# Performance work log

Hardware: AMD Instinct MI355X
Metric: run time of the kernel (lower is better)

The kernel has to match this reference:

```python
import jax, jax.numpy as jnp
import numpy as np

B, T, F = 64, 1024, 64  # F == K
K_FACTORS = 64
U = 256
GP_ELL = 10.0
GP_NOISE = 0.1


def setup_inputs() -> dict:
    key = jax.random.key(0)
    ks = jax.random.split(key, 5)
    inputs = jax.random.normal(ks[0], (B, T, F), dtype=jnp.float32)
    Wx = jax.random.normal(ks[1], (F, 4 * U), dtype=jnp.float32) * 0.05
    Wh = jax.random.normal(ks[2], (U, 4 * U), dtype=jnp.float32) * 0.05
    b = jnp.zeros((4 * U,), dtype=jnp.float32)
    Wd = jax.random.normal(ks[3], (U, 1), dtype=jnp.float32) * 0.05
    bd = jnp.zeros((1,), dtype=jnp.float32)
    return {"inputs": inputs, "Wx": Wx, "Wh": Wh, "b": b, "Wd": Wd, "bd": bd}


def _lstm(x, Wx, Wh, b):
    # x: (B, T, F) -> hidden sequence (B, T, U). Keras gate order: i, f, g(c), o.
    Bn = x.shape[0]
    Un = Wh.shape[0]
    x_t = jnp.swapaxes(x, 0, 1)  # (T, B, F)
    h0 = jnp.zeros((Bn, Un), x.dtype)
    c0 = jnp.zeros((Bn, Un), x.dtype)

    def step(carry, xt):
        h, c = carry
        z = xt @ Wx + h @ Wh + b  # (B, 4U)
        i, f, g, o = jnp.split(z, 4, axis=-1)
        i = jax.nn.sigmoid(i)
        f = jax.nn.sigmoid(f)
        g = jnp.tanh(g)
        o = jax.nn.sigmoid(o)
        c = f * c + i * g
        h = o * jnp.tanh(c)
        return (h, c), h

    _, hs = jax.lax.scan(step, (h0, c0), x_t)
    return jnp.swapaxes(hs, 0, 1)  # (B, T, U)


def _gp_posterior_mean(series_btf):
    # All series share the same time grid -> one (T,T) kernel solve for all.
    Tn = series_btf.shape[1]
    t = jnp.arange(Tn, dtype=series_btf.dtype)
    d = (t[:, None] - t[None, :]) / GP_ELL
    Kmat = jnp.exp(-0.5 * d * d)  # (T, T) RBF kernel
    A = Kmat + GP_NOISE * jnp.eye(Tn, dtype=series_btf.dtype)
    Y = jnp.swapaxes(series_btf, 0, 1).reshape(Tn, -1)  # (T, B*F)
    mean = Kmat @ jnp.linalg.solve(A, Y)  # (T, B*F)
    mean = mean.reshape(Tn, series_btf.shape[0], series_btf.shape[2])
    return jnp.swapaxes(mean, 0, 1)  # (B, T, F)


def reference(inputs, Wx, Wh, b, Wd, bd):
    # K identical LSTM+Dense branches (shared weights) -> compute once, broadcast.
    h = _lstm(inputs, Wx, Wh, b)          # (B, T, U)
    g = h @ Wd + bd                        # (B, T, 1)
    g_it = jnp.broadcast_to(g, (g.shape[0], g.shape[1], K_FACTORS))  # (B, T, K)

    # keras Attention (dot): scores = Q K^T, softmax over keys, out = scores @ V
    scores = jnp.einsum("btk,bsk->bts", g_it, g_it)  # (B, T, T)
    att = jnp.einsum("bts,bsk->btk", jax.nn.softmax(scores, axis=-1), g_it)
    attention_scores = jax.nn.softmax(att, axis=-1)  # extra softmax over K
    f_it = attention_scores * g_it

    r_it = _gp_posterior_mean(inputs)      # (B, T, F) with F == K
    u_it = f_it + r_it
    z_it = _gp_posterior_mean(u_it)        # (B, T, K)
    return z_it
```

## Files before the change

kernel.cpp:

```cpp
#include <hip/hip_runtime.h>

#define T_LEN 1024
#define LOG2E 1.4426950408889634f

typedef float f32x4 __attribute__((ext_vector_type(4)));
typedef unsigned long long u64;

__device__ __forceinline__ u64 pack8(float v0,float v1,float v2,float v3,
                                     float v4,float v5,float v6,float v7){
  int lo = __builtin_amdgcn_cvt_pk_fp8_f32(v0, v1, 0, false);
  lo = __builtin_amdgcn_cvt_pk_fp8_f32(v2, v3, lo, true);
  int hi = __builtin_amdgcn_cvt_pk_fp8_f32(v4, v5, 0, false);
  hi = __builtin_amdgcn_cvt_pk_fp8_f32(v6, v7, hi, true);
  return ((u64)(unsigned)hi << 32) | (unsigned)lo;
}

__device__ __forceinline__ float sigp(float y){
  return __builtin_amdgcn_rcpf(1.f + __builtin_amdgcn_exp2f(-y));
}

__global__ __launch_bounds__(512, 1) void lstm_kernel(
    const float* __restrict__ X, const float* __restrict__ Wx,
    const float* __restrict__ Wh, const float* __restrict__ Bias,
    const float* __restrict__ Wd, const float* __restrict__ Bd,
    float* __restrict__ g_out)
{
  __shared__ unsigned char wx_lds[64*1024];
  __shared__ unsigned char h_lds[8*512];
  __shared__ float g_part[8][16];

  const int tid = threadIdx.x;
  const int w = tid >> 6, l = tid & 63;
  const int l15 = l & 15, lhi = l >> 4;
  const int wg = blockIdx.x;

  for (int idx = tid; idx < 65536; idx += 512){
    int f = idx >> 10, n = idx & 1023;
    float s = ((n >> 8) == 2 ? 32.f : 16.f) * LOG2E;
    float v = Wx[idx] * s;
    int p = __builtin_amdgcn_cvt_pk_fp8_f32(v, v, 0, false);
    int mt = ((n >> 8) << 4) | ((n >> 4) & 15);
    wx_lds[mt*1024 + ((f >> 5) << 9) + (((f >> 3) & 3) << 7) + ((n & 15) << 3) + (f & 7)]
        = (unsigned char)(p & 0xff);
  }
  for (int idx = tid; idx < 4096; idx += 512) h_lds[idx] = 0;

  u64 whf[8][8];
  #pragma unroll
  for (int kt = 0; kt < 8; ++kt){
    #pragma unroll
    for (int g = 0; g < 4; ++g){
      float sA = (g == 2 ? 32.f : 16.f) * LOG2E;
      #pragma unroll
      for (int jj = 0; jj < 2; ++jj){
        int n = g*256 + w*32 + jj*16 + l15;
        int k0 = kt*32 + lhi*8;
        const float* p = Wh + (size_t)k0*1024 + n;
        whf[kt][g*2+jj] = pack8(p[0]*sA, p[1024]*sA, p[2048]*sA, p[3072]*sA,
                                p[4096]*sA, p[5120]*sA, p[6144]*sA, p[7168]*sA);
      }
    }
  }
  u64 wxb[8];
  #pragma unroll
  for (int g = 0; g < 4; ++g){
    float sA = (g == 2 ? 32.f : 16.f) * LOG2E;
    #pragma unroll
    for (int jj = 0; jj < 2; ++jj){
      int n = g*256 + w*32 + jj*16 + l15;
      wxb[g*2+jj] = (lhi == 0) ? pack8(Bias[n]*sA, 0,0,0,0,0,0,0) : 0ull;
    }
  }
  const u64 biasb = (lhi == 0) ? 0x58ull : 0ull;

  float wd_r[8];
  #pragma unroll
  for (int jj = 0; jj < 2; ++jj)
    #pragma unroll
    for (int r = 0; r < 4; ++r)
      wd_r[jj*4+r] = Wd[w*32 + jj*16 + lhi*4 + r];

  float c_r[8];
  #pragma unroll
  for (int i = 0; i < 8; ++i) c_r[i] = 0.f;
  const float bd0 = Bd[0];

  const float* xbase = X + (size_t)(wg*16 + l15)*65536;
  float4 xa = *(const float4*)(xbase + lhi*8);
  float4 xb = *(const float4*)(xbase + lhi*8 + 4);
  float4 xc = *(const float4*)(xbase + 32 + lhi*8);
  float4 xd = *(const float4*)(xbase + 36 + lhi*8);

  __syncthreads();

  const f32x4 z4 = {0.f, 0.f, 0.f, 0.f};
  const int hrd = lhi*128 + l15*8;
  const int hwr = w*512 + (lhi >> 1)*128 + l15*8 + (lhi & 1)*4;

  for (int t = 0; t < T_LEN; ++t){
    u64 hb[8];
    #pragma unroll
    for (int kt = 0; kt < 8; ++kt)
      hb[kt] = *(const u64*)&h_lds[kt*512 + hrd];

    f32x4 acc[8];
    #pragma unroll
    for (int m = 0; m < 8; ++m)
      acc[m] = __builtin_amdgcn_mfma_f32_16x16x32_fp8_fp8(
          (long)wxb[m], (long)biasb, z4, 0, 0, 0);

    #pragma unroll
    for (int kt = 0; kt < 8; ++kt)
      #pragma unroll
      for (int m = 0; m < 8; ++m)
        acc[m] = __builtin_amdgcn_mfma_f32_16x16x32_fp8_fp8(
            (long)whf[kt][m], (long)hb[kt], acc[m], 0, 0, 0);

    u64 ax0 = pack8(xa.x*16.f, xa.y*16.f, xa.z*16.f, xa.w*16.f,
                    xb.x*16.f, xb.y*16.f, xb.z*16.f, xb.w*16.f);
    u64 ax1 = pack8(xc.x*16.f, xc.y*16.f, xc.z*16.f, xc.w*16.f,
                    xd.x*16.f, xd.y*16.f, xd.z*16.f, xd.w*16.f);
    {
      int tn = (t < 1023) ? t + 1 : 1023;
      const float* xp = xbase + tn*64 + lhi*8;
      xa = *(const float4*)(xp);
      xb = *(const float4*)(xp + 4);
      xc = *(const float4*)(xp + 32);
      xd = *(const float4*)(xp + 36);
    }

    #pragma unroll
    for (int kt = 0; kt < 2; ++kt){
      const u64 bfr = kt ? ax1 : ax0;
      #pragma unroll
      for (int m = 0; m < 8; ++m){
        int mt = ((m >> 1) << 4) + w*2 + (m & 1);
        const u64 af = *(const u64*)&wx_lds[mt*1024 + (kt << 9) + (lhi << 7) + (l15 << 3)];
        acc[m] = __builtin_amdgcn_mfma_f32_16x16x32_fp8_fp8(
            (long)af, (long)bfr, acc[m], 0, 0, 0);
      }
    }

    float hsv[8];
    #pragma unroll
    for (int jj = 0; jj < 2; ++jj){
      #pragma unroll
      for (int r = 0; r < 4; ++r){
        float yi = acc[0+jj][r] * (1.f/256.f);
        float yf = acc[2+jj][r] * (1.f/256.f);
        float yg = acc[4+jj][r] * (1.f/256.f);
        float yo = acc[6+jj][r] * (1.f/256.f);
        float ig = sigp(yi);
        float fg = sigp(yf);
        float gg = 2.f*sigp(yg) - 1.f;
        float og = sigp(yo);
        float c = fmaf(fg, c_r[jj*4+r], ig*gg);
        c_r[jj*4+r] = c;
        float th = 2.f*sigp(c*(2.f*LOG2E)) - 1.f;
        hsv[jj*4+r] = og*th;
      }
    }

    float s = 0.f;
    #pragma unroll
    for (int i = 0; i < 8; ++i) s = fmaf(hsv[i], wd_r[i], s);
    s += __shfl_xor(s, 16, 64);
    s += __shfl_xor(s, 32, 64);

    __syncthreads();

    #pragma unroll
    for (int jj = 0; jj < 2; ++jj){
      int v0 = __builtin_amdgcn_cvt_pk_fp8_f32(hsv[jj*4+0]*16.f, hsv[jj*4+1]*16.f, 0, false);
      v0 = __builtin_amdgcn_cvt_pk_fp8_f32(hsv[jj*4+2]*16.f, hsv[jj*4+3]*16.f, v0, true);
      *(int*)&h_lds[hwr + jj*256] = v0;
    }
    if (l < 16) g_part[w][l15] = s;
    __syncthreads();

    if (w == 0 && l < 16){
      float gs = bd0;
      #pragma unroll
      for (int ww = 0; ww < 8; ++ww) gs += g_part[ww][l15];
      g_out[(size_t)(wg*16 + l15)*1024 + t] = gs;
    }
  }
}

__global__ __launch_bounds__(512) void cheb_kernel(float* __restrict__ cols)
{
  const int j0 = (blockIdx.x < 128) ? blockIdx.x : 512;
  __shared__ float dpad[64 + 1024 + 64];
  __shared__ float xv[1024];
  __shared__ float rv[1024];
  __shared__ float aband[65];
  const int tid = threadIdx.x;

  if (tid < 65){ float dd = tid*0.1f; aband[tid] = expf(-0.5f*dd*dd); }
  const float lmin = 0.0999f, lmax = 25.3f;
  const float th = 0.5f*(lmax+lmin), de = 0.5f*(lmax-lmin);
  const float s1 = th/de;
  float rho = 1.f/s1;

  for (int t = tid; t < 1024; t += 512){
    float r0 = (t == j0) ? 1.f : 0.f;
    xv[t] = 0.f; rv[t] = r0; dpad[64+t] = r0/th;
  }
  if (tid < 64){ dpad[tid] = 0.f; dpad[64+1024+tid] = 0.f; }
  __syncthreads();

  for (int it = 0; it < 80; ++it){
    float ad[2];
    #pragma unroll
    for (int h = 0; h < 2; ++h){
      int t = tid + h*512;
      const float* dp = &dpad[64+t];
      float a = 1.1f * dp[0];
      #pragma unroll 8
      for (int jj = 1; jj <= 48; ++jj) a = fmaf(aband[jj], dp[jj] + dp[-jj], a);
      ad[h] = a;
    }
    float rhon = 1.f/(2.f*s1 - rho);
    __syncthreads();
    #pragma unroll
    for (int h = 0; h < 2; ++h){
      int t = tid + h*512;
      float dold = dpad[64+t];
      xv[t] += dold;
      float r = rv[t] - ad[h];
      rv[t] = r;
      dpad[64+t] = rhon*rho*dold + (2.f*rhon/de)*r;
    }
    rho = rhon;
    __syncthreads();
  }
  for (int t = tid; t < 1024; t += 512) cols[(size_t)blockIdx.x*1024 + t] = xv[t];
}

template<int ADDF>
__global__ __launch_bounds__(256) void apply_kernel(
    const float* __restrict__ in, const float* __restrict__ cols,
    const float* __restrict__ gbuf, float* __restrict__ out)
{
  const int b  = blockIdx.x >> 2;
  const int c0 = (blockIdx.x & 3) * 16;
  __shared__ float xt[1024*16];
  __shared__ float st[257];

  const float* src = in + (size_t)b*65536 + c0;
  for (int idx = threadIdx.x; idx < 4096; idx += 256){
    int t = idx >> 2, q = idx & 3;
    *(float4*)(&xt[t*16 + q*4]) = *(const float4*)(src + t*64 + q*4);
  }
  for (int i = threadIdx.x; i < 257; i += 256) st[i] = cols[128*1024 + 384 + i];
  __syncthreads();

  float* dst = out + (size_t)b*65536 + c0;
  for (int idx = threadIdx.x; idx < 768*16; idx += 256){
    int t = 128 + (idx >> 4), c = idx & 15;
    float a = 0.f;
    #pragma unroll 8
    for (int j = 0; j < 257; ++j) a = fmaf(st[j], xt[(t-128+j)*16 + c], a);
    float v = xt[t*16+c] - 0.1f*a;
    if (ADDF) v += gbuf[b*1024+t]*0.015625f;
    dst[t*64 + c] = v;
  }
  for (int idx = threadIdx.x; idx < 256*16; idx += 256){
    int tb = idx >> 4, c = idx & 15;
    float a = 0.f;
    int t, tt;
    if (tb < 128){
      t = tb; tt = tb;
      for (int s = 0; s < 384; ++s) a = fmaf(cols[(size_t)tt*1024 + s], xt[s*16 + c], a);
    } else {
      t = 896 + (tb - 128); tt = 1023 - t;
      for (int s = 0; s < 384; ++s) a = fmaf(cols[(size_t)tt*1024 + s], xt[(1023-s)*16 + c], a);
    }
    float v = xt[t*16+c] - 0.1f*a;
    if (ADDF) v += gbuf[b*1024+t]*0.015625f;
    dst[t*64 + c] = v;
  }
}

extern "C" void kernel_launch(void* const* d_in, const int* in_sizes, int n_in,
                              void* d_out, int out_size, void* d_ws, size_t ws_size,
                              hipStream_t stream)
{
  const float* X    = (const float*)d_in[0];
  const float* Wx   = (const float*)d_in[1];
  const float* Wh   = (const float*)d_in[2];
  const float* Bias = (const float*)d_in[3];
  const float* Wd   = (const float*)d_in[4];
  const float* Bd   = (const float*)d_in[5];
  float* out = (float*)d_out;
  char* ws = (char*)d_ws;

  float* g    = (float*)ws;
  float* cols = (float*)(ws + (256<<10));

  hipLaunchKernelGGL(lstm_kernel, dim3(4),   dim3(512), 0, stream,
                     X, Wx, Wh, Bias, Wd, Bd, g);
  hipLaunchKernelGGL(cheb_kernel, dim3(129), dim3(512), 0, stream, cols);
  hipLaunchKernelGGL((apply_kernel<1>), dim3(256), dim3(256), 0, stream, X,   cols, g, out);
  hipLaunchKernelGGL((apply_kernel<0>), dim3(256), dim3(256), 0, stream, out, cols, g, out);
}
```

Baseline: 3.293 ms.

## Switch LSTM to int8 MFMA, fuse Chebyshev solve into LSTM launch, retile apply

The LSTM recurrence moves from fp8 16x16x32 MFMA to int8 16x16x64 MFMA with fixed-point scales. Part of Wh now lives in LDS to cut register pressure, and h is double-buffered so each step needs only one barrier. The Chebyshev column solve runs in extra blocks of the same launch, overlapping with the serial LSTM instead of running as a separate kernel. The apply kernel is retiled with register sliding windows, a padded LDS layout and transposed boundary columns. This adds int8 quantization error and a much larger, riskier code change.

```diff
diff --git a/kernel.cpp b/kernel.cpp
--- a/kernel.cpp
+++ b/kernel.cpp
@@ -2,283 +2,358 @@
 
 #define T_LEN 1024
 #define LOG2E 1.4426950408889634f
-
-typedef float f32x4 __attribute__((ext_vector_type(4)));
-typedef unsigned long long u64;
-
-__device__ __forceinline__ u64 pack8(float v0,float v1,float v2,float v3,
-                                     float v4,float v5,float v6,float v7){
-  int lo = __builtin_amdgcn_cvt_pk_fp8_f32(v0, v1, 0, false);
-  lo = __builtin_amdgcn_cvt_pk_fp8_f32(v2, v3, lo, true);
-  int hi = __builtin_amdgcn_cvt_pk_fp8_f32(v4, v5, 0, false);
-  hi = __builtin_amdgcn_cvt_pk_fp8_f32(v6, v7, hi, true);
-  return ((u64)(unsigned)hi << 32) | (unsigned)lo;
-}
+#define SW 423.0f
+#define SX 21.0f
+
+typedef int v4i __attribute__((ext_vector_type(4)));
 
 __device__ __forceinline__ float sigp(float y){
   return __builtin_amdgcn_rcpf(1.f + __builtin_amdgcn_exp2f(-y));
 }
-
-__global__ __launch_bounds__(512, 1) void lstm_kernel(
+__device__ __forceinline__ int packq4(float a, float b, float c, float d, float s){
+  int q0 = (int)rintf(a*s), q1 = (int)rintf(b*s);
+  int q2 = (int)rintf(c*s), q3 = (int)rintf(d*s);
+  return (q0&255) | ((q1&255)<<8) | ((q2&255)<<16) | (q3<<24);
+}
+
+__global__ __launch_bounds__(512, 2) void fat_kernel(
     const float* __restrict__ X, const float* __restrict__ Wx,
     const float* __restrict__ Wh, const float* __restrict__ Bias,
     const float* __restrict__ Wd, const float* __restrict__ Bd,
-    float* __restrict__ g_out)
+    float* __restrict__ g_out, float* __restrict__ colsT,
+    float* __restrict__ st1)
 {
-  __shared__ unsigned char wx_lds[64*1024];
-  __shared__ unsigned char h_lds[8*512];
-  __shared__ float g_part[8][16];
+  __shared__ __attribute__((aligned(16))) unsigned char wx_lds[64*1024];
+  __shared__ __attribute__((aligned(16))) unsigned char whl_lds[64*1024];
+  __shared__ __attribute__((aligned(16))) unsigned char h_lds[2][16][272];
+  __shared__ float g_part[2][8][16];
+  __shared__ float cb_dpad[64 + 1024 + 64];
+  __shared__ float cb_xv[1024];
+  __shared__ float cb_rv[1024];
+  __shared__ float cb_aband[65];
 
   const int tid = threadIdx.x;
-  const int w = tid >> 6, l = tid & 63;
-  const int l15 = l & 15, lhi = l >> 4;
-  const int wg = blockIdx.x;
-
-  for (int idx = tid; idx < 65536; idx += 512){
-    int f = idx >> 10, n = idx & 1023;
-    float s = ((n >> 8) == 2 ? 32.f : 16.f) * LOG2E;
-    float v = Wx[idx] * s;
-    int p = __builtin_amdgcn_cvt_pk_fp8_f32(v, v, 0, false);
-    int mt = ((n >> 8) << 4) | ((n >> 4) & 15);
-    wx_lds[mt*1024 + ((f >> 5) << 9) + (((f >> 3) & 3) << 7) + ((n & 15) << 3) + (f & 7)]
-        = (unsigned char)(p & 0xff);
+
+  if (blockIdx.x < 4){
+    const int w = tid >> 6, l = tid & 63;
+    const int l15 = l & 15, lhi = l >> 4;
+    const int wg = blockIdx.x;
+
+    for (int slot = tid; slot < 4096; slot += 512){
+      int mt = slot >> 6, ln = slot & 63;
+      int n = mt*16 + (ln & 15);
+      const float* wp = Wx + (size_t)((ln >> 4)*16)*1024 + n;
+      int* dst = (int*)&wx_lds[slot*16];
+      #pragma unroll
+      for (int d = 0; d < 4; ++d)
+        dst[d] = packq4(wp[(d*4+0)*1024], wp[(d*4+1)*1024],
+                        wp[(d*4+2)*1024], wp[(d*4+3)*1024], SW);
+    }
+    for (int slot = tid; slot < 4096; slot += 512){
+      int tile = slot >> 8, kb = (slot >> 6) & 3, ln = slot & 63;
+      int n = 768 + (tile >> 1)*32 + (tile & 1)*16 + (ln & 15);
+      const float* wp = Wh + (size_t)(kb*64 + (ln >> 4)*16)*1024 + n;
+      int* dst = (int*)&whl_lds[((tile*4 + kb)*64 + ln)*16];
+      #pragma unroll
+      for (int d = 0; d < 4; ++d)
+        dst[d] = packq4(wp[(d*4+0)*1024], wp[(d*4+1)*1024],
+                        wp[(d*4+2)*1024], wp[(d*4+3)*1024], SW);
+    }
+    for (int idx = tid; idx < 2176; idx += 512) ((int*)h_lds)[idx] = 0;
+
+    v4i whf[4][6];
+    #pragma unroll
+    for (int m = 0; m < 6; ++m){
+      int g = m >> 1, jj = m & 1;
+      int n = g*256 + w*32 + jj*16 + l15;
+      #pragma unroll
+      for (int kb = 0; kb < 4; ++kb){
+        const float* wp = Wh + (size_t)(kb*64 + lhi*16)*1024 + n;
+        v4i f;
+        #pragma unroll
+        for (int d = 0; d < 4; ++d)
+          f[d] = packq4(wp[(d*4+0)*1024], wp[(d*4+1)*1024],
+                        wp[(d*4+2)*1024], wp[(d*4+3)*1024], SW);
+        whf[kb][m] = f;
+      }
+    }
+    int ab0[8];
+    #pragma unroll
+    for (int m = 0; m < 8; ++m){
+      int g = m >> 1, jj = m & 1;
+      int n = g*256 + w*32 + jj*16 + l15;
+      ab0[m] = (lhi == 0) ? ((int)rintf(Bias[n]*SW) & 255) : 0;
+    }
+    v4i bb = { (lhi == 0) ? 127 : 0, 0, 0, 0 };
+    const v4i zero4 = {0,0,0,0};
+
+    float wd_r[8];
+    #pragma unroll
+    for (int jj = 0; jj < 2; ++jj)
+      #pragma unroll
+      for (int r = 0; r < 4; ++r)
+        wd_r[jj*4+r] = Wd[w*32 + jj*16 + lhi*4 + r];
+
+    float c_r[8];
+    #pragma unroll
+    for (int i = 0; i < 8; ++i) c_r[i] = 0.f;
+    const float bd0 = Bd[0];
+    const float cHs = LOG2E/(SW*127.f);
+    const float cXs = LOG2E/(SW*SX);
+
+    const float* xrow = X + (size_t)(wg*16 + l15)*65536 + lhi*16;
+    float4 xf0 = *(const float4*)(xrow + 0);
+    float4 xf1 = *(const float4*)(xrow + 4);
+    float4 xf2 = *(const float4*)(xrow + 8);
+    float4 xf3 = *(const float4*)(xrow + 12);
+    v4i xq;
+    xq[0] = packq4(xf0.x, xf0.y, xf0.z, xf0.w, SX);
+    xq[1] = packq4(xf1.x, xf1.y, xf1.z, xf1.w, SX);
+    xq[2] = packq4(xf2.x, xf2.y, xf2.z, xf2.w, SX);
+    xq[3] = packq4(xf3.x, xf3.y, xf3.z, xf3.w, SX);
+    xf0 = *(const float4*)(xrow + 64 + 0);
+    xf1 = *(const float4*)(xrow + 64 + 4);
+    xf2 = *(const float4*)(xrow + 64 + 8);
+    xf3 = *(const float4*)(xrow + 64 + 12);
+
+    __syncthreads();
+
+    int p = 0;
+    for (int t = 0; t < T_LEN; ++t){
+      v4i accH[8], accX[8];
+      #pragma unroll
+      for (int m = 0; m < 8; ++m){
+        v4i ab = { ab0[m], 0, 0, 0 };
+        accH[m] = __builtin_amdgcn_mfma_i32_16x16x64_i8(ab, bb, zero4, 0, 0, 0);
+      }
+      #pragma unroll
+      for (int kb = 0; kb < 4; ++kb){
+        v4i hbk = *(const v4i*)&h_lds[p][l15][kb*64 + lhi*16];
+        #pragma unroll
+        for (int m = 0; m < 6; ++m)
+          accH[m] = __builtin_amdgcn_mfma_i32_16x16x64_i8(whf[kb][m], hbk, accH[m], 0, 0, 0);
+        #pragma unroll
+        for (int m = 6; m < 8; ++m){
+          v4i wf = *(const v4i*)&whl_lds[(((w*2 + (m&1))*4 + kb)*64 + l)*16];
+          accH[m] = __builtin_amdgcn_mfma_i32_16x16x64_i8(wf, hbk, accH[m], 0, 0, 0);
+        }
+      }
+      #pragma unroll
+      for (int m = 0; m < 8; ++m){
+        int mt = (m >> 1)*16 + w*2 + (m & 1);
+        v4i wxf = *(const v4i*)&wx_lds[(mt*64 + l)*16];
+        accX[m] = __builtin_amdgcn_mfma_i32_16x16x64_i8(wxf, xq, zero4, 0, 0, 0);
+      }
+
+      v4i xqn;
+      xqn[0] = packq4(xf0.x, xf0.y, xf0.z, xf0.w, SX);
+      xqn[1] = packq4(xf1.x, xf1.y, xf1.z, xf1.w, SX);
+      xqn[2] = packq4(xf2.x, xf2.y, xf2.z, xf2.w, SX);
+      xqn[3] = packq4(xf3.x, xf3.y, xf3.z, xf3.w, SX);
+      {
+        int tn = (t < 1022) ? t + 2 : 1023;
+        const float* xp = xrow + (size_t)tn*64;
+        xf0 = *(const float4*)(xp + 0);
+        xf1 = *(const float4*)(xp + 4);
+        xf2 = *(const float4*)(xp + 8);
+        xf3 = *(const float4*)(xp + 12);
+      }
+
+      float hsv[8];
+      #pragma unroll
+      for (int jj = 0; jj < 2; ++jj){
+        #pragma unroll
+        for (int r = 0; r < 4; ++r){
+          float yi = (float)accH[0+jj][r]*cHs      + (float)accX[0+jj][r]*cXs;
+          float yf = (float)accH[2+jj][r]*cHs      + (float)accX[2+jj][r]*cXs;
+          float yg = (float)accH[4+jj][r]*(2.f*cHs)+ (float)accX[4+jj][r]*(2.f*cXs);
+          float yo = (float)accH[6+jj][r]*cHs      + (float)accX[6+jj][r]*cXs;
+          float ig = sigp(yi);
+          float fg = sigp(yf);
+          float gg = 2.f*sigp(yg) - 1.f;
+          float og = sigp(yo);
+          float c = fmaf(fg, c_r[jj*4+r], ig*gg);
+          c_r[jj*4+r] = c;
+          float th = 2.f*sigp(c*(2.f*LOG2E)) - 1.f;
+          hsv[jj*4+r] = og*th;
+        }
+      }
+
+      float s = 0.f;
+      #pragma unroll
+      for (int i = 0; i < 8; ++i) s = fmaf(hsv[i], wd_r[i], s);
+      s += __shfl_xor(s, 16, 64);
+      s += __shfl_xor(s, 32, 64);
+
+      #pragma unroll
+      for (int jj = 0; jj < 2; ++jj){
+        int dw = packq4(hsv[jj*4+0], hsv[jj*4+1], hsv[jj*4+2], hsv[jj*4+3], 127.f);
+        *(int*)&h_lds[p^1][l15][(w*2+jj)*16 + lhi*4] = dw;
+      }
+      if (l < 16) g_part[p][w][l15] = s;
+      xq = xqn;
+
+      __syncthreads();
+
+      if (w == 0 && l < 16){
+        float gs = bd0;
+        #pragma unroll
+        for (int ww = 0; ww < 8; ++ww) gs += g_part[p][ww][l15];
+        g_out[(size_t)(wg*16 + l15)*1024 + t] = gs;
+      }
+      p ^= 1;
+    }
+  } else {
+    const int cidx = blockIdx.x - 4;
+    const int j0 = (cidx < 128) ? cidx : 512;
+
+    if (tid < 65){ float dd = tid*0.1f; cb_aband[tid] = expf(-0.5f*dd*dd); }
+    const float lmin = 0.0999f, lmax = 25.3f;
+    const float th = 0.5f*(lmax+lmin), de = 0.5f*(lmax-lmin);
+    const float s1 = th/de;
+    float rho = 1.f/s1;
+
+    for (int t = tid; t < 1024; t += 512){
+      float r0 = (t == j0) ? 1.f : 0.f;
+      cb_xv[t] = 0.f; cb_rv[t] = r0; cb_dpad[64+t] = r0/th;
+    }
+    if (tid < 64){ cb_dpad[tid] = 0.f; cb_dpad[64+1024+tid] = 0.f; }
+    __syncthreads();
+
+    for (int it = 0; it < 80; ++it){
+      float ad[2];
+      #pragma unroll
+      for (int h = 0; h < 2; ++h){
+        int t = tid + h*512;
+        const float* dp = &cb_dpad[64+t];
+        float a = 1.1f * dp[0];
+        #pragma unroll 8
+        for (int jj = 1; jj <= 48; ++jj) a = fmaf(cb_aband[jj], dp[jj] + dp[-jj], a);
+        ad[h] = a;
+      }
+      float rhon = 1.f/(2.f*s1 - rho);
+      __syncthreads();
+      #pragma unroll
+      for (int h = 0; h < 2; ++h){
+        int t = tid + h*512;
+        float dold = cb_dpad[64+t];
+        cb_xv[t] += dold;
+        float r = cb_rv[t] - ad[h];
+        cb_rv[t] = r;
+        cb_dpad[64+t] = rhon*rho*dold + (2.f*rhon/de)*r;
+      }
+      rho = rhon;
+      __syncthreads();
+    }
+    if (cidx == 128){
+      for (int i = tid; i < 257; i += 512) st1[i] = cb_xv[384 + i];
+    } else {
+      for (int s = tid; s < 1024; s += 512) colsT[(size_t)s*128 + cidx] = cb_xv[s];
+    }
   }
-  for (int idx = tid; idx < 4096; idx += 512) h_lds[idx] = 0;
-
-  u64 whf[8][8];
-  #pragma unroll
-  for (int kt = 0; kt < 8; ++kt){
-    #pragma unroll
-    for (int g = 0; g < 4; ++g){
-      float sA = (g == 2 ? 32.f : 16.f) * LOG2E;
-      #pragma unroll
-      for (int jj = 0; jj < 2; ++jj){
-        int n = g*256 + w*32 + jj*16 + l15;
-        int k0 = kt*32 + lhi*8;
-        const float* p = Wh + (size_t)k0*1024 + n;
-        whf[kt][g*2+jj] = pack8(p[0]*sA, p[1024]*sA, p[2048]*sA, p[3072]*sA,
-                                p[4096]*sA, p[5120]*sA, p[6144]*sA, p[7168]*sA);
-      }
-    }
-  }
-  u64 wxb[8];
-  #pragma unroll
-  for (int g = 0; g < 4; ++g){
-    float sA = (g == 2 ? 32.f : 16.f) * LOG2E;
-    #pragma unroll
-    for (int jj = 0; jj < 2; ++jj){
-      int n = g*256 + w*32 + jj*16 + l15;
-      wxb[g*2+jj] = (lhi == 0) ? pack8(Bias[n]*sA, 0,0,0,0,0,0,0) : 0ull;
-    }
-  }
-  const u64 biasb = (lhi == 0) ? 0x58ull : 0ull;
-
-  float wd_r[8];
-  #pragma unroll
-  for (int jj = 0; jj < 2; ++jj)
-    #pragma unroll
-    for (int r = 0; r < 4; ++r)
-      wd_r[jj*4+r] = Wd[w*32 + jj*16 + lhi*4 + r];
-
-  float c_r[8];
-  #pragma unroll
-  for (int i = 0; i < 8; ++i) c_r[i] = 0.f;
-  const float bd0 = Bd[0];
-
-  const float* xbase = X + (size_t)(wg*16 + l15)*65536;
-  float4 xa = *(const float4*)(xbase + lhi*8);
-  float4 xb = *(const float4*)(xbase + lhi*8 + 4);
-  float4 xc = *(const float4*)(xbase + 32 + lhi*8);
-  float4 xd = *(const float4*)(xbase + 36 + lhi*8);
-
-  __syncthreads();
-
-  const f32x4 z4 = {0.f, 0.f, 0.f, 0.f};
-  const int hrd = lhi*128 + l15*8;
-  const int hwr = w*512 + (lhi >> 1)*128 + l15*8 + (lhi & 1)*4;
-
-  for (int t = 0; t < T_LEN; ++t){
-    u64 hb[8];
-    #pragma unroll
-    for (int kt = 0; kt < 8; ++kt)
-      hb[kt] = *(const u64*)&h_lds[kt*512 + hrd];
-
-    f32x4 acc[8];
-    #pragma unroll
-    for (int m = 0; m < 8; ++m)
-      acc[m] = __builtin_amdgcn_mfma_f32_16x16x32_fp8_fp8(
-          (long)wxb[m], (long)biasb, z4, 0, 0, 0);
-
-    #pragma unroll
-    for (int kt = 0; kt < 8; ++kt)
-      #pragma unroll
-      for (int m = 0; m < 8; ++m)
-        acc[m] = __builtin_amdgcn_mfma_f32_16x16x32_fp8_fp8(
-            (long)whf[kt][m], (long)hb[kt], acc[m], 0, 0, 0);
-
-    u64 ax0 = pack8(xa.x*16.f, xa.y*16.f, xa.z*16.f, xa.w*16.f,
-                    xb.x*16.f, xb.y*16.f, xb.z*16.f, xb.w*16.f);
-    u64 ax1 = pack8(xc.x*16.f, xc.y*16.f, xc.z*16.f, xc.w*16.f,
-                    xd.x*16.f, xd.y*16.f, xd.z*16.f, xd.w*16.f);
-    {
-      int tn = (t < 1023) ? t + 1 : 1023;
-      const float* xp = xbase + tn*64 + lhi*8;
-      xa = *(const float4*)(xp);
-      xb = *(const float4*)(xp + 4);
-      xc = *(const float4*)(xp + 32);
-      xd = *(const float4*)(xp + 36);
-    }
-
-    #pragma unroll
-    for (int kt = 0; kt < 2; ++kt){
-      const u64 bfr = kt ? ax1 : ax0;
-      #pragma unroll
-      for (int m = 0; m < 8; ++m){
-        int mt = ((m >> 1) << 4) + w*2 + (m & 1);
-        const u64 af = *(const u64*)&wx_lds[mt*1024 + (kt << 9) + (lhi << 7) + (l15 << 3)];
-        acc[m] = __builtin_amdgcn_mfma_f32_16x16x32_fp8_fp8(
-            (long)af, (long)bfr, acc[m], 0, 0, 0);
-      }
-    }
-
-    float hsv[8];
-    #pragma unroll
-    for (int jj = 0; jj < 2; ++jj){
-      #pragma unroll
-      for (int r = 0; r < 4; ++r){
-        float yi = acc[0+jj][r] * (1.f/256.f);
-        float yf = acc[2+jj][r] * (1.f/256.f);
-        float yg = acc[4+jj][r] * (1.f/256.f);
-        float yo = acc[6+jj][r] * (1.f/256.f);
-        float ig = sigp(yi);
-        float fg = sigp(yf);
-        float gg = 2.f*sigp(yg) - 1.f;
-        float og = sigp(yo);
-        float c = fmaf(fg, c_r[jj*4+r], ig*gg);
-        c_r[jj*4+r] = c;
-        float th = 2.f*sigp(c*(2.f*LOG2E)) - 1.f;
-        hsv[jj*4+r] = og*th;
-      }
-    }
-
-    float s = 0.f;
-    #pragma unroll
-    for (int i = 0; i < 8; ++i) s = fmaf(hsv[i], wd_r[i], s);
-    s += __shfl_xor(s, 16, 64);
-    s += __shfl_xor(s, 32, 64);
-
-    __syncthreads();
-
-    #pragma unroll
-    for (int jj = 0; jj < 2; ++jj){
-      int v0 = __builtin_amdgcn_cvt_pk_fp8_f32(hsv[jj*4+0]*16.f, hsv[jj*4+1]*16.f, 0, false);
-      v0 = __builtin_amdgcn_cvt_pk_fp8_f32(hsv[jj*4+2]*16.f, hsv[jj*4+3]*16.f, v0, true);
-      *(int*)&h_lds[hwr + jj*256] = v0;
-    }
-    if (l < 16) g_part[w][l15] = s;
-    __syncthreads();
-
-    if (w == 0 && l < 16){
-      float gs = bd0;
-      #pragma unroll
-      for (int ww = 0; ww < 8; ++ww) gs += g_part[ww][l15];
-      g_out[(size_t)(wg*16 + l15)*1024 + t] = gs;
-    }
-  }
-}
-
-__global__ __launch_bounds__(512) void cheb_kernel(float* __restrict__ cols)
-{
-  const int j0 = (blockIdx.x < 128) ? blockIdx.x : 512;
-  __shared__ float dpad[64 + 1024 + 64];
-  __shared__ float xv[1024];
-  __shared__ float rv[1024];
-  __shared__ float aband[65];
-  const int tid = threadIdx.x;
-
-  if (tid < 65){ float dd = tid*0.1f; aband[tid] = expf(-0.5f*dd*dd); }
-  const float lmin = 0.0999f, lmax = 25.3f;
-  const float th = 0.5f*(lmax+lmin), de = 0.5f*(lmax-lmin);
-  const float s1 = th/de;
-  float rho = 1.f/s1;
-
-  for (int t = tid; t < 1024; t += 512){
-    float r0 = (t == j0) ? 1.f : 0.f;
-    xv[t] = 0.f; rv[t] = r0; dpad[64+t] = r0/th;
-  }
-  if (tid < 64){ dpad[tid] = 0.f; dpad[64+1024+tid] = 0.f; }
-  __syncthreads();
-
-  for (int it = 0; it < 80; ++it){
-    float ad[2];
-    #pragma unroll
-    for (int h = 0; h < 2; ++h){
-      int t = tid + h*512;
-      const float* dp = &dpad[64+t];
-      float a = 1.1f * dp[0];
-      #pragma unroll 8
-      for (int jj = 1; jj <= 48; ++jj) a = fmaf(aband[jj], dp[jj] + dp[-jj], a);
-      ad[h] = a;
-    }
-    float rhon = 1.f/(2.f*s1 - rho);
-    __syncthreads();
-    #pragma unroll
-    for (int h = 0; h < 2; ++h){
-      int t = tid + h*512;
-      float dold = dpad[64+t];
-      xv[t] += dold;
-      float r = rv[t] - ad[h];
-      rv[t] = r;
-      dpad[64+t] = rhon*rho*dold + (2.f*rhon/de)*r;
-    }
-    rho = rhon;
-    __syncthreads();
-  }
-  for (int t = tid; t < 1024; t += 512) cols[(size_t)blockIdx.x*1024 + t] = xv[t];
 }
 
 template<int ADDF>
 __global__ __launch_bounds__(256) void apply_kernel(
-    const float* __restrict__ in, const float* __restrict__ cols,
-    const float* __restrict__ gbuf, float* __restrict__ out)
+    const float* __restrict__ in, const float* __restrict__ colsT,
+    const float* __restrict__ st1, const float* __restrict__ gbuf,
+    float* __restrict__ out)
 {
   const int b  = blockIdx.x >> 2;
   const int c0 = (blockIdx.x & 3) * 16;
-  __shared__ float xt[1024*16];
-  __shared__ float st[257];
+  __shared__ float xt[1040*17];
+  __shared__ float stc[260];
 
   const float* src = in + (size_t)b*65536 + c0;
-  for (int idx = threadIdx.x; idx < 4096; idx += 256){
-    int t = idx >> 2, q = idx & 3;
-    *(float4*)(&xt[t*16 + q*4]) = *(const float4*)(src + t*64 + q*4);
+  for (int idx = threadIdx.x; idx < 16384; idx += 256){
+    int t = idx >> 4, c = idx & 15;
+    xt[t*17 + c] = src[t*64 + c];
   }
-  for (int i = threadIdx.x; i < 257; i += 256) st[i] = cols[128*1024 + 384 + i];
+  for (int i = threadIdx.x; i < 257; i += 256) stc[i] = st1[i];
   __syncthreads();
 
   float* dst = out + (size_t)b*65536 + c0;
-  for (int idx = threadIdx.x; idx < 768*16; idx += 256){
-    int t = 128 + (idx >> 4), c = idx & 15;
-    float a = 0.f;
-    #pragma unroll 8
-    for (int j = 0; j < 257; ++j) a = fmaf(st[j], xt[(t-128+j)*16 + c], a);
-    float v = xt[t*16+c] - 0.1f*a;
-    if (ADDF) v += gbuf[b*1024+t]*0.015625f;
-    dst[t*64 + c] = v;
+
+  for (int task = threadIdx.x; task < 1536; task += 256){
+    int tb = task >> 4, c = task & 15;
+    int base = tb*8;
+    float acc[8];
+    #pragma unroll
+    for (int i = 0; i < 8; ++i) acc[i] = 0.f;
+    float wreg[16];
+    #pragma unroll
+    for (int q = 0; q < 16; ++q) wreg[q] = xt[(base+q)*17 + c];
+
+    for (int jo = 0; jo < 256; jo += 8){
+      float sv[8];
+      *(float4*)(sv)   = *(const float4*)&stc[jo];
+      *(float4*)(sv+4) = *(const float4*)&stc[jo+4];
+      #pragma unroll
+      for (int jj = 0; jj < 8; ++jj){
+        float s = sv[jj];
+        #pragma unroll
+        for (int i = 0; i < 8; ++i) acc[i] = fmaf(s, wreg[jj+i], acc[i]);
+      }
+      #pragma unroll
+      for (int q = 0; q < 8; ++q) wreg[q] = wreg[q+8];
+      #pragma unroll
+      for (int q = 0; q < 8; ++q) wreg[8+q] = xt[(base+jo+16+q)*17 + c];
+    }
+    #pragma unroll
+    for (int i = 0; i < 8; ++i) acc[i] = fmaf(stc[256], wreg[i], acc[i]);
+
+    #pragma unroll
+    for (int i = 0; i < 8; ++i){
+      int t = 128 + base + i;
+      float v = xt[t*17 + c] - 0.1f*acc[i];
+      if (ADDF) v += gbuf[b*1024 + t]*0.015625f;
+      dst[t*64 + c] = v;
+    }
   }
-  for (int idx = threadIdx.x; idx < 256*16; idx += 256){
-    int tb = idx >> 4, c = idx & 15;
-    float a = 0.f;
-    int t, tt;
-    if (tb < 128){
-      t = tb; tt = tb;
-      for (int s = 0; s < 384; ++s) a = fmaf(cols[(size_t)tt*1024 + s], xt[s*16 + c], a);
+
+  for (int task = threadIdx.x; task < 512; task += 256){
+    int tb = task >> 4, c = task & 15;
+    float acc[8];
+    #pragma unroll
+    for (int i = 0; i < 8; ++i) acc[i] = 0.f;
+    if (tb < 16){
+      int t0 = tb*8;
+      for (int s = 0; s < 384; ++s){
+        float xv = xt[s*17 + c];
+        float4 cv0 = *(const float4*)&colsT[(size_t)s*128 + t0];
+        float4 cv1 = *(const float4*)&colsT[(size_t)s*128 + t0 + 4];
+        acc[0] = fmaf(cv0.x, xv, acc[0]); acc[1] = fmaf(cv0.y, xv, acc[1]);
+        acc[2] = fmaf(cv0.z, xv, acc[2]); acc[3] = fmaf(cv0.w, xv, acc[3]);
+        acc[4] = fmaf(cv1.x, xv, acc[4]); acc[5] = fmaf(cv1.y, xv, acc[5]);
+        acc[6] = fmaf(cv1.z, xv, acc[6]); acc[7] = fmaf(cv1.w, xv, acc[7]);
+      }
+      #pragma unroll
+      for (int i = 0; i < 8; ++i){
+        int t = t0 + i;
+        float v = xt[t*17 + c] - 0.1f*acc[i];
+        if (ADDF) v += gbuf[b*1024 + t]*0.015625f;
+        dst[t*64 + c] = v;
+      }
     } else {
-      t = 896 + (tb - 128); tt = 1023 - t;
-      for (int s = 0; s < 384; ++s) a = fmaf(cols[(size_t)tt*1024 + s], xt[(1023-s)*16 + c], a);
-    }
-    float v = xt[t*16+c] - 0.1f*a;
-    if (ADDF) v += gbuf[b*1024+t]*0.015625f;
-    dst[t*64 + c] = v;
+      int t0 = 896 + (tb - 16)*8;
+      int ttb = 1016 - t0;
+      for (int s = 0; s < 384; ++s){
+        float xv = xt[(1023 - s)*17 + c];
+        float4 cv0 = *(const float4*)&colsT[(size_t)s*128 + ttb];
+        float4 cv1 = *(const float4*)&colsT[(size_t)s*128 + ttb + 4];
+        acc[7] = fmaf(cv0.x, xv, acc[7]); acc[6] = fmaf(cv0.y, xv, acc[6]);
+        acc[5] = fmaf(cv0.z, xv, acc[5]); acc[4] = fmaf(cv0.w, xv, acc[4]);
+        acc[3] = fmaf(cv1.x, xv, acc[3]); acc[2] = fmaf(cv1.y, xv, acc[2]);
+        acc[1] = fmaf(cv1.z, xv, acc[1]); acc[0] = fmaf(cv1.w, xv, acc[0]);
+      }
+      #pragma unroll
+      for (int i = 0; i < 8; ++i){
+        int t = t0 + i;
+        float v = xt[t*17 + c] - 0.1f*acc[i];
+        if (ADDF) v += gbuf[b*1024 + t]*0.015625f;
+        dst[t*64 + c] = v;
+      }
+    }
   }
 }
 
@@ -295,12 +370,14 @@
   float* out = (float*)d_out;
   char* ws = (char*)d_ws;
 
-  float* g    = (float*)ws;
-  float* cols = (float*)(ws + (256<<10));
-
-  hipLaunchKernelGGL(lstm_kernel, dim3(4),   dim3(512), 0, stream,
-                     X, Wx, Wh, Bias, Wd, Bd, g);
-  hipLaunchKernelGGL(cheb_kernel, dim3(129), dim3(512), 0, stream, cols);
-  hipLaunchKernelGGL((apply_kernel<1>), dim3(256), dim3(256), 0, stream, X,   cols, g, out);
-  hipLaunchKernelGGL((apply_kernel<0>), dim3(256), dim3(256), 0, stream, out, cols, g, out);
-}
+  float* g     = (float*)ws;
+  float* colsT = (float*)(ws + (256<<10));
+  float* st1   = (float*)(ws + (768<<10));
+
+  hipLaunchKernelGGL(fat_kernel, dim3(133), dim3(512), 0, stream,
+                     X, Wx, Wh, Bias, Wd, Bd, g, colsT, st1);
+  hipLaunchKernelGGL((apply_kernel<1>), dim3(256), dim3(256), 0, stream,
+                     X, colsT, st1, g, out);
+  hipLaunchKernelGGL((apply_kernel<0>), dim3(256), dim3(256), 0, stream,
+                     out, colsT, st1, g, out);
+}
```

Result: faster. 2.786 ms (-15.4%).
